# Performance work log

Hardware: AMD Instinct MI355X
Metric: run time of the kernel (lower is better)

## Reference

```python
import jax, jax.numpy as jnp
import numpy as np

B, C, IN, OUT = 2048, 64, 512, 512


def setup_inputs() -> dict:
    key = jax.random.key(0)
    k1, k2, k3 = jax.random.split(key, 3)
    x = jax.random.normal(k1, (B, IN), dtype=jnp.float32)
    index = jax.random.randint(k2, (B,), 0, C, dtype=jnp.int64)
    # kaiming_uniform-ish init: bound = sqrt(6 / ((1 + 5) * fan_in)) = 1/sqrt(fan_in)
    bound = 1.0 / np.sqrt(IN)
    weight = jax.random.uniform(k3, (C, OUT, IN), dtype=jnp.float32,
                                minval=-bound, maxval=bound)
    return {"input": x, "index": index, "weight": weight}


def reference(input, index, weight):
    # weight: (C, OUT, IN); index: (B,); input: (B, IN)
    w = weight[index]                      # (B, OUT, IN) gathered per-sample matrix
    return jnp.einsum('boi,bi->bo', w, input)  # batched matvec -> (B, OUT)
```

## Files before the change

### kernel.cpp

```cpp
#include <hip/hip_runtime.h>


constexpr int Bsz  = 2048;
constexpr int Ccnt = 64;
constexpr int INF  = 512;
constexpr int OUTF = 512;
constexpr int THREADS = 256;
constexpr int OT = 16;
constexpr int NBLK = Ccnt * (OUTF / OT);

typedef __attribute__((ext_vector_type(8))) short bf16x8;
typedef __attribute__((ext_vector_type(4))) float f32x4;

#if __has_builtin(__builtin_amdgcn_cvt_pk_bf16_f32)
typedef __attribute__((ext_vector_type(2))) __bf16 bf16x2_t;
__device__ __forceinline__ int cvt2i(float a, float b) {
    union { bf16x2_t v; int i; } u;
    u.v = __builtin_amdgcn_cvt_pk_bf16_f32(a, b);
    return u.i;
}
#else
__device__ __forceinline__ unsigned f2bf(float f) {
    union { float f; unsigned u; } v; v.f = f;
    return (v.u + 0x7FFFu + ((v.u >> 16) & 1u)) >> 16;
}
__device__ __forceinline__ int cvt2i(float a, float b) {
    return (int)(f2bf(a) | (f2bf(b) << 16));
}
#endif

__device__ __forceinline__ bf16x8 cvt8(float4 a, float4 b) {
    union { bf16x8 v; int i[4]; } u;
    u.i[0] = cvt2i(a.x, a.y);
    u.i[1] = cvt2i(a.z, a.w);
    u.i[2] = cvt2i(b.x, b.y);
    u.i[3] = cvt2i(b.z, b.w);
    return u.v;
}

__device__ __forceinline__ void gld_lds16(const float* g, float* l) {
    __builtin_amdgcn_global_load_lds(
        (const __attribute__((address_space(1))) float*)g,
        (__attribute__((address_space(3))) float*)l, 16, 0, 0);
}

__global__ __launch_bounds__(THREADS, 3)
void switching_linear_kernel(const float* __restrict__ x,
                             const int* __restrict__ idx,
                             const float* __restrict__ w,
                             float* __restrict__ out) {
    __shared__ float Wl[OT * INF];
    __shared__ unsigned short list[Bsz];
    __shared__ int ls_n;
    __shared__ float red[4][3][4][64];

    const int tid  = threadIdx.x;
    const int wave = tid >> 6;
    const int lane = tid & 63;
    const int c  = blockIdx.x >> 5;
    const int o0 = (blockIdx.x & 31) * OT;

    if (tid == 0) ls_n = 0;
    __syncthreads();

    const float* wc = w + (size_t)c * OUTF * INF + (size_t)o0 * INF;
#pragma unroll
    for (int i = 0; i < 8; ++i) {
        const int inst = wave * 8 + i;
        const int r = inst >> 1;
        const int h = inst & 1;
        const int p = r & 7;
        const float* src = wc + (size_t)r * INF + (h * 64 + (lane ^ p)) * 4;
        gld_lds16(src, &Wl[inst * 256]);
    }

    int my[8];
#pragma unroll
    for (int i = 0; i < 8; ++i) my[i] = idx[tid + i * THREADS];
#pragma unroll
    for (int i = 0; i < 8; ++i)
        if (my[i] == c) list[atomicAdd(&ls_n, 1)] = (unsigned short)(tid + i * THREADS);

    __syncthreads();
    const int n = ls_n;
    if (n == 0) return;

    const int mrow = lane & 15;
    const int quad = lane >> 4;
    const int k0   = wave * (INF / 4);
    const int p    = mrow & 7;

    bf16x8 wf[4];
#pragma unroll
    for (int t = 0; t < 4; ++t) {
        const int gb = (k0 >> 2) + t * 8 + quad * 2;
        float4 a0 = *(const float4*)&Wl[mrow * INF + ((gb)     ^ p) * 4];
        float4 a1 = *(const float4*)&Wl[mrow * INF + ((gb + 1) ^ p) * 4];
        wf[t] = cvt8(a0, a1);
    }

    for (int s0 = 0; s0 < n; s0 += 64) {
        const int rem = n - s0;
        const int ng  = rem >= 64 ? 4 : (rem + 15) >> 4;

        f32x4 acc[4];
#pragma unroll
        for (int g = 0; g < 4; ++g) acc[g] = (f32x4){0.f, 0.f, 0.f, 0.f};

#pragma unroll 2
        for (int g = 0; g < ng; ++g) {
            const int s = s0 + g * 16 + mrow;
            const bool v = (s < n);
            const float* bp = x + (size_t)(v ? (int)list[s] : 0) * INF + k0 + quad * 8;
            bf16x8 xf[4];
            if (v) {
#pragma unroll
                for (int i = 0; i < 4; ++i) {
                    float4 b0 = *(const float4*)(bp + i * 32);
                    float4 b1 = *(const float4*)(bp + i * 32 + 4);
                    xf[i] = cvt8(b0, b1);
                }
            } else {
#pragma unroll
                for (int i = 0; i < 4; ++i) xf[i] = (bf16x8){0,0,0,0,0,0,0,0};
            }
#pragma unroll
            for (int i = 0; i < 4; ++i)
                acc[g] = __builtin_amdgcn_mfma_f32_16x16x32_bf16(wf[i], xf[i], acc[g], 0, 0, 0);
        }

        if (wave != 0) {
#pragma unroll
            for (int g = 0; g < 4; ++g) {
                if (g < ng) {
#pragma unroll
                    for (int j = 0; j < 4; ++j) red[g][wave - 1][j][lane] = acc[g][j];
                }
            }
        }
        __syncthreads();
        if (wave == 0) {
#pragma unroll
            for (int g = 0; g < 4; ++g) {
                if (g < ng) {
                    const int s = s0 + g * 16 + mrow;
                    if (s < n) {
                        f32x4 a = acc[g];
#pragma unroll
                        for (int wv2 = 0; wv2 < 3; ++wv2)
#pragma unroll
                            for (int j = 0; j < 4; ++j) a[j] += red[g][wv2][j][lane];
                        float* dst = out + (size_t)list[s] * OUTF + o0 + quad * 4;
                        *(float4*)dst = make_float4(a[0], a[1], a[2], a[3]);
                    }
                }
            }
        }
        __syncthreads();
    }
}

extern "C" void kernel_launch(void* const* d_in, const int* in_sizes, int n_in,
                              void* d_out, int out_size, void* d_ws, size_t ws_size,
                              hipStream_t stream) {
    const float* x   = (const float*)d_in[0];
    const int*   idx = (const int*)d_in[1];
    const float* w   = (const float*)d_in[2];
    float* out = (float*)d_out;

    switching_linear_kernel<<<dim3(NBLK), dim3(THREADS), 0, stream>>>(x, idx, w, out);
}
```

Measured before the change: 112.9 us.

## Process four output tiles per block with double-buffered weight staging

Each block now handles four 16-row output tiles of one expert instead of one. The index scan and list build are done once per block rather than once per tile. The next weight tile is prefetched into a second LDS buffer while the current one is computed, block IDs are remapped across XCDs, and the cross-wave reduction is split into two-group chunks with a lighter barrier. Shared memory grows and occupancy drops to 2 blocks per SM, the grid has fewer blocks, and reloading x once per output tile costs more cache traffic.

```diff
diff --git a/kernel.cpp b/kernel.cpp
--- a/kernel.cpp
+++ b/kernel.cpp
@@ -6,8 +6,9 @@
 constexpr int INF  = 512;
 constexpr int OUTF = 512;
 constexpr int THREADS = 256;
-constexpr int OT = 16;
-constexpr int NBLK = Ccnt * (OUTF / OT);
+constexpr int OT  = 16;
+constexpr int TPB = 4;
+constexpr int NBLK = Ccnt * (OUTF / (OT * TPB));
 
 typedef __attribute__((ext_vector_type(8))) short bf16x8;
 typedef __attribute__((ext_vector_type(4))) float f32x4;
@@ -44,35 +45,49 @@
         (__attribute__((address_space(3))) float*)l, 16, 0, 0);
 }
 
-__global__ __launch_bounds__(THREADS, 3)
-void switching_linear_kernel(const float* __restrict__ x,
-                             const int* __restrict__ idx,
-                             const float* __restrict__ w,
-                             float* __restrict__ out) {
-    __shared__ float Wl[OT * INF];
-    __shared__ unsigned short list[Bsz];
-    __shared__ int ls_n;
-    __shared__ float red[4][3][4][64];
-
-    const int tid  = threadIdx.x;
-    const int wave = tid >> 6;
-    const int lane = tid & 63;
-    const int c  = blockIdx.x >> 5;
-    const int o0 = (blockIdx.x & 31) * OT;
-
-    if (tid == 0) ls_n = 0;
-    __syncthreads();
-
-    const float* wc = w + (size_t)c * OUTF * INF + (size_t)o0 * INF;
+__device__ __forceinline__ void barrier_lgkm() {
+    asm volatile("s_waitcnt lgkmcnt(0)" ::: "memory");
+    __builtin_amdgcn_s_barrier();
+    asm volatile("" ::: "memory");
+}
+
+__device__ __forceinline__ void stage_tile(const float* wt, float* dst,
+                                           int wave, int lane) {
 #pragma unroll
     for (int i = 0; i < 8; ++i) {
         const int inst = wave * 8 + i;
         const int r = inst >> 1;
         const int h = inst & 1;
         const int p = r & 7;
-        const float* src = wc + (size_t)r * INF + (h * 64 + (lane ^ p)) * 4;
-        gld_lds16(src, &Wl[inst * 256]);
+        const float* src = wt + (size_t)r * INF + (h * 64 + (lane ^ p)) * 4;
+        gld_lds16(src, dst + inst * 256);
     }
+}
+
+__global__ __launch_bounds__(THREADS, 2)
+void switching_linear_kernel(const float* __restrict__ x,
+                             const int* __restrict__ idx,
+                             const float* __restrict__ w,
+                             float* __restrict__ out) {
+    __shared__ float Wl[2][OT * INF];
+    __shared__ unsigned short list[Bsz];
+    __shared__ int ls_n;
+    __shared__ float red[2][3][4][64];
+
+    const int tid  = threadIdx.x;
+    const int wave = tid >> 6;
+    const int lane = tid & 63;
+
+    const int bid   = ((int)blockIdx.x & 7) * (NBLK / 8) + ((int)blockIdx.x >> 3);
+    const int c     = bid >> 3;
+    const int obase = (bid & 7) * (OT * TPB);
+
+    if (tid == 0) ls_n = 0;
+    __syncthreads();
+
+    const float* wc = w + (size_t)c * OUTF * INF + (size_t)obase * INF;
+
+    stage_tile(wc, Wl[0], wave, lane);
 
     int my[8];
 #pragma unroll
@@ -80,83 +95,98 @@
 #pragma unroll
     for (int i = 0; i < 8; ++i)
         if (my[i] == c) list[atomicAdd(&ls_n, 1)] = (unsigned short)(tid + i * THREADS);
-
-    __syncthreads();
-    const int n = ls_n;
-    if (n == 0) return;
 
     const int mrow = lane & 15;
     const int quad = lane >> 4;
     const int k0   = wave * (INF / 4);
     const int p    = mrow & 7;
 
-    bf16x8 wf[4];
-#pragma unroll
-    for (int t = 0; t < 4; ++t) {
-        const int gb = (k0 >> 2) + t * 8 + quad * 2;
-        float4 a0 = *(const float4*)&Wl[mrow * INF + ((gb)     ^ p) * 4];
-        float4 a1 = *(const float4*)&Wl[mrow * INF + ((gb + 1) ^ p) * 4];
-        wf[t] = cvt8(a0, a1);
-    }
-
-    for (int s0 = 0; s0 < n; s0 += 64) {
-        const int rem = n - s0;
-        const int ng  = rem >= 64 ? 4 : (rem + 15) >> 4;
-
-        f32x4 acc[4];
-#pragma unroll
-        for (int g = 0; g < 4; ++g) acc[g] = (f32x4){0.f, 0.f, 0.f, 0.f};
-
-#pragma unroll 2
-        for (int g = 0; g < ng; ++g) {
-            const int s = s0 + g * 16 + mrow;
-            const bool v = (s < n);
-            const float* bp = x + (size_t)(v ? (int)list[s] : 0) * INF + k0 + quad * 8;
-            bf16x8 xf[4];
-            if (v) {
-#pragma unroll
-                for (int i = 0; i < 4; ++i) {
-                    float4 b0 = *(const float4*)(bp + i * 32);
-                    float4 b1 = *(const float4*)(bp + i * 32 + 4);
-                    xf[i] = cvt8(b0, b1);
-                }
-            } else {
-#pragma unroll
-                for (int i = 0; i < 4; ++i) xf[i] = (bf16x8){0,0,0,0,0,0,0,0};
-            }
-#pragma unroll
-            for (int i = 0; i < 4; ++i)
-                acc[g] = __builtin_amdgcn_mfma_f32_16x16x32_bf16(wf[i], xf[i], acc[g], 0, 0, 0);
+    int n = 0;
+
+    for (int ot = 0; ot < TPB; ++ot) {
+        __syncthreads();
+        if (ot == 0) {
+            n = ls_n;
+            if (n == 0) return;
         }
-
-        if (wave != 0) {
+        if (ot + 1 < TPB)
+            stage_tile(wc + (size_t)((ot + 1) * OT) * INF, Wl[(ot + 1) & 1],
+                       wave, lane);
+
+        const float* Wb = Wl[ot & 1];
+        const int o0 = obase + ot * OT;
+
+        bf16x8 wf[4];
+#pragma unroll
+        for (int t = 0; t < 4; ++t) {
+            const int gb = (k0 >> 2) + t * 8 + quad * 2;
+            float4 a0 = *(const float4*)&Wb[mrow * INF + ((gb)     ^ p) * 4];
+            float4 a1 = *(const float4*)&Wb[mrow * INF + ((gb + 1) ^ p) * 4];
+            wf[t] = cvt8(a0, a1);
+        }
+
+        for (int s0 = 0; s0 < n; s0 += 64) {
+            const int rem = n - s0;
+            const int ng  = rem >= 64 ? 4 : (rem + 15) >> 4;
+
+            f32x4 acc[4];
+#pragma unroll
+            for (int g = 0; g < 4; ++g) acc[g] = (f32x4){0.f, 0.f, 0.f, 0.f};
+
 #pragma unroll
             for (int g = 0; g < 4; ++g) {
                 if (g < ng) {
-#pragma unroll
-                    for (int j = 0; j < 4; ++j) red[g][wave - 1][j][lane] = acc[g][j];
+                    const int s  = s0 + g * 16 + mrow;
+                    const int sc = s < n ? s : n - 1;
+                    const float* bp = x + (size_t)list[sc] * INF + k0 + quad * 8;
+#pragma unroll
+                    for (int i = 0; i < 4; ++i) {
+                        float4 b0 = *(const float4*)(bp + i * 32);
+                        float4 b1 = *(const float4*)(bp + i * 32 + 4);
+                        acc[g] = __builtin_amdgcn_mfma_f32_16x16x32_bf16(
+                                     wf[i], cvt8(b0, b1), acc[g], 0, 0, 0);
+                    }
+                }
+            }
+
+#pragma unroll
+            for (int r0 = 0; r0 < 4; r0 += 2) {
+                if (r0 < ng) {
+                    if (wave != 0) {
+#pragma unroll
+                        for (int g = 0; g < 2; ++g) {
+                            if (r0 + g < ng) {
+#pragma unroll
+                                for (int j = 0; j < 4; ++j)
+                                    red[g][wave - 1][j][lane] = acc[r0 + g][j];
+                            }
+                        }
+                    }
+                    barrier_lgkm();
+                    if (wave == 0) {
+#pragma unroll
+                        for (int g = 0; g < 2; ++g) {
+                            if (r0 + g < ng) {
+                                const int s = s0 + (r0 + g) * 16 + mrow;
+                                if (s < n) {
+                                    f32x4 a = acc[r0 + g];
+#pragma unroll
+                                    for (int wv2 = 0; wv2 < 3; ++wv2)
+#pragma unroll
+                                        for (int j = 0; j < 4; ++j)
+                                            a[j] += red[g][wv2][j][lane];
+                                    float* dst = out + (size_t)list[s] * OUTF
+                                                     + o0 + quad * 4;
+                                    *(float4*)dst = make_float4(a[0], a[1],
+                                                                a[2], a[3]);
+                                }
+                            }
+                        }
+                    }
+                    barrier_lgkm();
                 }
             }
         }
-        __syncthreads();
-        if (wave == 0) {
-#pragma unroll
-            for (int g = 0; g < 4; ++g) {
-                if (g < ng) {
-                    const int s = s0 + g * 16 + mrow;
-                    if (s < n) {
-                        f32x4 a = acc[g];
-#pragma unroll
-                        for (int wv2 = 0; wv2 < 3; ++wv2)
-#pragma unroll
-                            for (int j = 0; j < 4; ++j) a[j] += red[g][wv2][j][lane];
-                        float* dst = out + (size_t)list[s] * OUTF + o0 + quad * 4;
-                        *(float4*)dst = make_float4(a[0], a[1], a[2], a[3]);
-                    }
-                }
-            }
-        }
-        __syncthreads();
     }
 }
 
```

After: 116.1 us. +2.8%, slower.
